# Kernel optimization log

Measured on AMD Instinct MI355X. Metric: run time of the kernel, lower is better.

The kernel has to match this reference:

```python
import jax, jax.numpy as jnp
import numpy as np

R, K = 16, 64  # rel_size (heads), key_size (head dim)
LN_EPS = 1e-5


def apply_rope(x, pos):
    # pos: [B,S,1,K], halves are sin/cos; x: [B,S,R,K]
    sin, cos = jnp.split(pos, 2, axis=-1)
    x0, x1 = jnp.split(x, 2, axis=-1)
    return jnp.concatenate([x0 * cos - x1 * sin, x0 * sin + x1 * cos], axis=-1)


def setup_inputs() -> dict:
    key = jax.random.key(0)
    ks = jax.random.split(key, 6)
    B, S, H = 2, 2048, 1024
    x = jax.random.normal(ks[0], (B, S, H), dtype=jnp.float32)
    pos = jax.random.uniform(ks[1], (B, S, 1, K), dtype=jnp.float32)
    W_qkv = jax.random.normal(ks[2], (H, R * K * 3), dtype=jnp.float32) * (H ** -0.5)
    b_qkv = jax.random.normal(ks[3], (R * K * 3,), dtype=jnp.float32) * 0.02
    W_out = jax.random.normal(ks[4], (R * K, H), dtype=jnp.float32) * ((R * K) ** -0.5)
    b_out = jax.random.normal(ks[5], (H,), dtype=jnp.float32) * 0.02
    ln_g = jnp.ones((H,), dtype=jnp.float32)
    ln_b = jnp.zeros((H,), dtype=jnp.float32)
    return {"x": x, "pos": pos, "W_qkv": W_qkv, "b_qkv": b_qkv,
            "W_out": W_out, "b_out": b_out, "ln_g": ln_g, "ln_b": ln_b}


def reference(x, pos, W_qkv, b_qkv, W_out, b_out, ln_g, ln_b):
    B, S, H = x.shape
    qkv = (x @ W_qkv + b_qkv).reshape(B, S, R, 3 * K)
    q, k, v = jnp.split(qkv, 3, axis=-1)  # each [B,S,R,K]
    k = k / jnp.linalg.norm(k, axis=-1, keepdims=True)
    q = apply_rope(q, pos)
    k = apply_rope(k, pos)
    # SDPA with scale=1 (as in the original call)
    scores = jnp.einsum('bqhd,bkhd->bhqk', q, k)
    attn = jax.nn.softmax(scores, axis=-1)
    ctx = jnp.einsum('bhqk,bkhd->bqhd', attn, v).reshape(B, S, R * K)
    postx = ctx @ W_out + b_out
    y = x + postx
    mu = jnp.mean(y, axis=-1, keepdims=True)
    var = jnp.mean(jnp.square(y - mu), axis=-1, keepdims=True)
    return (y - mu) * jax.lax.rsqrt(var + LN_EPS) * ln_g + ln_b
```

## Files before the change

### kernel.cpp

```cpp
#include <hip/hip_runtime.h>


#define B_   2
#define S_   2048
#define H_   1024
#define R_   16
#define BS_  (B_*S_)
#define NQKV 3072
#define LOG2E 1.44269504088896f

typedef float    floatx4 __attribute__((ext_vector_type(4)));
typedef _Float16 half8   __attribute__((ext_vector_type(8)));
typedef _Float16 half4   __attribute__((ext_vector_type(4)));
typedef __fp16   fp16x2  __attribute__((ext_vector_type(2)));

#if __has_builtin(__builtin_amdgcn_exp2f)
#define EXP2(x) __builtin_amdgcn_exp2f(x)
#else
#define EXP2(x) exp2f(x)
#endif

__device__ __forceinline__ void gl_lds16(const _Float16* g, _Float16* l) {
    __builtin_amdgcn_global_load_lds(
        (const __attribute__((address_space(1))) unsigned int*)g,
        (__attribute__((address_space(3))) unsigned int*)l, 16, 0, 0);
}

__global__ __launch_bounds__(256) void prep0_kernel(
    const float* __restrict__ x, _Float16* __restrict__ x_h,
    const float* __restrict__ W_qkv, _Float16* __restrict__ wqkv_t,
    const float* __restrict__ W_out, _Float16* __restrict__ wout_t)
{
    __shared__ float tile[32][33];
    int bid = blockIdx.x, tid = threadIdx.x;
    if (bid < 4096) {
        int i = bid * 1024 + tid * 4;
        float4 v = *(const float4*)(x + i);
        half4 h;
        h.x = (_Float16)v.x; h.y = (_Float16)v.y;
        h.z = (_Float16)v.z; h.w = (_Float16)v.w;
        *(half4*)(x_h + i) = h;
        return;
    }
    const float* in; _Float16* out; int rows, cols, bx, by;
    if (bid < 7168) {
        int t = bid - 4096;
        in = W_qkv; out = wqkv_t; rows = H_; cols = NQKV;
        bx = t % 96; by = t / 96;
    } else {
        int t = bid - 7168;
        in = W_out; out = wout_t; rows = H_; cols = H_;
        bx = t & 31; by = t >> 5;
    }
    int cx = bx * 32, ry = by * 32;
    int tx = tid & 31, ty = tid >> 5;
#pragma unroll
    for (int i = 0; i < 32; i += 8)
        tile[ty + i][tx] = in[(size_t)(ry + ty + i) * cols + cx + tx];
    __syncthreads();
#pragma unroll
    for (int i = 0; i < 32; i += 8)
        out[(size_t)(cx + ty + i) * rows + ry + tx] = (_Float16)tile[tx][ty + i];
}

__global__ __launch_bounds__(256) void gemm_f16_mfma(
    const _Float16* __restrict__ A, const _Float16* __restrict__ Bt,
    const float* __restrict__ bias, _Float16* __restrict__ Ch,
    int M, int N, int Kd)
{
    __shared__ _Float16 Als[2][4096];
    __shared__ _Float16 Bls[2][4096];
    int tid  = threadIdx.x;
    int lane = tid & 63, w = tid >> 6;
    int wr = w >> 1, wc = w & 1;
    int fr = lane & 15, fq = lane >> 4;

    int nbx = gridDim.x;
    int orig = blockIdx.x + nbx * blockIdx.y;
    int nwg  = nbx * gridDim.y;
    int swz  = (nwg & 7) ? orig : ((orig & 7) * (nwg >> 3) + (orig >> 3));
    int bx = swz % nbx, by = swz / nbx;
    int m0 = by * 128, n0 = bx * 128;

    floatx4 acc[4][4] = {};

    const _Float16* ga[2]; const _Float16* gb[2];
    int loff[2];
#pragma unroll
    for (int i2 = 0; i2 < 2; ++i2) {
        int ch = 2 * w + i2;
        int row = ch * 16 + (lane >> 2), col = (lane & 3) * 8;
        ga[i2] = A  + (size_t)(m0 + row) * Kd + col;
        gb[i2] = Bt + (size_t)(n0 + row) * Kd + col;
        loff[i2] = ch * 512;
    }

    int nIter = Kd >> 5;
#pragma unroll
    for (int i2 = 0; i2 < 2; ++i2) {
        gl_lds16(ga[i2], &Als[0][loff[i2]]);
        gl_lds16(gb[i2], &Bls[0][loff[i2]]);
    }

    for (int it = 0; it < nIter; ++it) {
        int cur = it & 1;
        __syncthreads();
        if (it + 1 < nIter) {
            int k1 = (it + 1) << 5;
#pragma unroll
            for (int i2 = 0; i2 < 2; ++i2) {
                gl_lds16(ga[i2] + k1, &Als[cur ^ 1][loff[i2]]);
                gl_lds16(gb[i2] + k1, &Bls[cur ^ 1][loff[i2]]);
            }
        }
        const _Float16* Ab = Als[cur];
        const _Float16* Bb = Bls[cur];
        half8 af[4], bf[4];
#pragma unroll
        for (int i = 0; i < 4; ++i)
            af[i] = *(const half8*)(Ab + (wr * 64 + i * 16 + fr) * 32 + fq * 8);
#pragma unroll
        for (int j = 0; j < 4; ++j)
            bf[j] = *(const half8*)(Bb + (wc * 64 + j * 16 + fr) * 32 + fq * 8);
#pragma unroll
        for (int i = 0; i < 4; ++i)
#pragma unroll
            for (int j = 0; j < 4; ++j)
                acc[i][j] = __builtin_amdgcn_mfma_f32_16x16x32_f16(
                    af[i], bf[j], acc[i][j], 0, 0, 0);
    }

#pragma unroll
    for (int i = 0; i < 4; ++i)
#pragma unroll
        for (int j = 0; j < 4; ++j)
#pragma unroll
            for (int r2 = 0; r2 < 4; ++r2) {
                int row = m0 + wr * 64 + i * 16 + fq * 4 + r2;
                int col = n0 + wc * 64 + j * 16 + fr;
                Ch[(size_t)row * N + col] = (_Float16)(acc[i][j][r2] + bias[col]);
            }
}

__global__ __launch_bounds__(256) void gemm64_f16_mfma(
    const _Float16* __restrict__ A, const _Float16* __restrict__ Bt,
    const float* __restrict__ bias, const float* __restrict__ resid,
    float* __restrict__ Cf, int M, int N, int Kd)
{
    __shared__ _Float16 Als[2][2048];
    __shared__ _Float16 Bls[2][2048];
    int tid = threadIdx.x, lane = tid & 63, w = tid >> 6;
    int wr = w >> 1, wc = w & 1;
    int fr = lane & 15, fq = lane >> 4;

    int nbx = gridDim.x;
    int orig = blockIdx.x + nbx * blockIdx.y;
    int nwg  = nbx * gridDim.y;
    int swz  = (nwg & 7) ? orig : ((orig & 7) * (nwg >> 3) + (orig >> 3));
    int bx = swz % nbx, by = swz / nbx;
    int m0 = by * 64, n0 = bx * 64;

    floatx4 acc[2][2] = {};

    int srow = w * 16 + (lane >> 2), scol = (lane & 3) * 8;
    const _Float16* ga = A  + (size_t)(m0 + srow) * Kd + scol;
    const _Float16* gb = Bt + (size_t)(n0 + srow) * Kd + scol;
    int loff = w * 512;

    int nIter = Kd >> 5;
    gl_lds16(ga, &Als[0][loff]);
    gl_lds16(gb, &Bls[0][loff]);

    for (int it = 0; it < nIter; ++it) {
        int cur = it & 1;
        __syncthreads();
        if (it + 1 < nIter) {
            int k1 = (it + 1) << 5;
            gl_lds16(ga + k1, &Als[cur ^ 1][loff]);
            gl_lds16(gb + k1, &Bls[cur ^ 1][loff]);
        }
        const _Float16* Ab = Als[cur];
        const _Float16* Bb = Bls[cur];
        half8 af[2], bf[2];
#pragma unroll
        for (int i = 0; i < 2; ++i)
            af[i] = *(const half8*)(Ab + (wr * 32 + i * 16 + fr) * 32 + fq * 8);
#pragma unroll
        for (int j = 0; j < 2; ++j)
            bf[j] = *(const half8*)(Bb + (wc * 32 + j * 16 + fr) * 32 + fq * 8);
#pragma unroll
        for (int i = 0; i < 2; ++i)
#pragma unroll
            for (int j = 0; j < 2; ++j)
                acc[i][j] = __builtin_amdgcn_mfma_f32_16x16x32_f16(
                    af[i], bf[j], acc[i][j], 0, 0, 0);
    }

#pragma unroll
    for (int i = 0; i < 2; ++i)
#pragma unroll
        for (int j = 0; j < 2; ++j)
#pragma unroll
            for (int r2 = 0; r2 < 4; ++r2) {
                int row = m0 + wr * 32 + i * 16 + fq * 4 + r2;
                int col = n0 + wc * 32 + j * 16 + fr;
                Cf[(size_t)row * N + col] =
                    acc[i][j][r2] + bias[col] + resid[(size_t)row * N + col];
            }
}

__global__ __launch_bounds__(256) void prep1_kernel(
    const _Float16* __restrict__ qkvh, const float* __restrict__ pos,
    _Float16* __restrict__ qt, _Float16* __restrict__ kt,
    _Float16* __restrict__ vt2)
{
    __shared__ float tile[64][65];
    int head = blockIdx.x, tau = blockIdx.y;
    int s0 = tau * 64;
    int b = head >> 4, rh = head & 15;
    int lane = threadIdx.x & 63, w = threadIdx.x >> 6;

#pragma unroll
    for (int si = w; si < 64; si += 4)
        tile[si][lane] =
            (float)qkvh[(size_t)(b * S_ + s0 + si) * NQKV + rh * 192 + 128 + lane];
    __syncthreads();
    {
        int P = lane;
        int op = P >> 3;
        int hi = (P >> 2) & 1, lo = P & 3;
#pragma unroll
        for (int d = w; d < 64; d += 4) {
            int ol = op ^ (d & 7);
            int key = 32 * (ol >> 2) + 16 * hi + 4 * (ol & 3) + lo;
            vt2[(((size_t)head * 32 + tau) * 64 + d) * 64 + P] = (_Float16)tile[key][d];
        }
    }

    for (int i = 0; i < 16; ++i) {
        int s = s0 + w * 16 + i;
        int bs = b * S_ + s;
        const _Float16* base = qkvh + (size_t)bs * NQKV + rh * 192;
        float qv = (float)base[lane];
        float kv = (float)base[64 + lane];

        float ss = kv * kv;
#pragma unroll
        for (int off = 32; off > 0; off >>= 1) ss += __shfl_xor(ss, off);
        kv *= rsqrtf(ss);

        int j = lane & 31;
        float sn = pos[(size_t)bs * 64 + j];
        float cs = pos[(size_t)bs * 64 + 32 + j];
        float qp = __shfl_xor(qv, 32);
        float kp = __shfl_xor(kv, 32);
        float qo, ko;
        if (lane < 32) { qo = qv * cs - qp * sn; ko = kv * cs - kp * sn; }
        else           { qo = qp * sn + qv * cs; ko = kp * sn + kv * cs; }

        size_t oidx = ((size_t)head * S_ + s) * 64 + lane;
        qt[oidx] = (_Float16)(qo * LOG2E);
        kt[oidx] = (_Float16)ko;
    }
}

__global__ __launch_bounds__(256) void attn_mfma_kernel(
    const _Float16* __restrict__ qt, const _Float16* __restrict__ kt,
    const _Float16* __restrict__ vt2,
    _Float16* __restrict__ opart, float* __restrict__ lpart)
{
    __shared__ _Float16 Kls[2][4096];
    __shared__ _Float16 Vls[2][4096];

    int orig = blockIdx.x + 16 * blockIdx.y + 512 * blockIdx.z;
    int swz  = (orig & 7) * 128 + (orig >> 3);
    int q0   = (swz & 15) * 128;
    int head = (swz >> 4) & 31;
    int ks   = swz >> 9;

    int b = head >> 4, rh = head & 15;
    int tid = threadIdx.x, lane = tid & 63, w = tid >> 6;
    int g = lane >> 4, c = lane & 15;

    half8 qf[2][2];
    float mL[2], l_s[2] = {0.f, 0.f};
#pragma unroll
    for (int qg = 0; qg < 2; ++qg) {
        const _Float16* qp =
            qt + ((size_t)head * S_ + q0 + w * 32 + qg * 16 + c) * 64 + 8 * g;
        qf[qg][0] = *(const half8*)qp;
        qf[qg][1] = *(const half8*)(qp + 32);
        float qq = 0.f;
#pragma unroll
        for (int i = 0; i < 8; ++i) {
            float a = (float)qf[qg][0][i], b2 = (float)qf[qg][1][i];
            qq += a * a + b2 * b2;
        }
        qq += __shfl_xor(qq, 16);
        qq += __shfl_xor(qq, 32);
        mL[qg] = sqrtf(qq);
    }

    floatx4 o_acc[2][4] = {};

    const _Float16* kg[2]; const _Float16* vg[2];
    int loff[2];
#pragma unroll
    for (int i2 = 0; i2 < 2; ++i2) {
        int ch = 2 * w + i2;
        int krow = ch * 8 + (lane >> 3);
        int koct = (lane & 7) ^ (lane >> 3);
        kg[i2] = kt + ((size_t)head * S_ + krow) * 64 + koct * 8;
        vg[i2] = vt2 + ((size_t)head * 32) * 4096 + ch * 512 + lane * 8;
        loff[i2] = ch * 512;
    }

    int co = c & 7;
    int jbase = ks << 4;

#pragma unroll
    for (int i2 = 0; i2 < 2; ++i2) {
        gl_lds16(kg[i2] + (size_t)jbase * 4096, &Kls[0][loff[i2]]);
        gl_lds16(vg[i2] + (size_t)jbase * 4096, &Vls[0][loff[i2]]);
    }

    for (int jt = 0; jt < 16; ++jt) {
        int cur = jt & 1;
        __syncthreads();
        if (jt + 1 < 16) {
            size_t joff = (size_t)(jbase + jt + 1) * 4096;
#pragma unroll
            for (int i2 = 0; i2 < 2; ++i2) {
                gl_lds16(kg[i2] + joff, &Kls[cur ^ 1][loff[i2]]);
                gl_lds16(vg[i2] + joff, &Vls[cur ^ 1][loff[i2]]);
            }
        }
        const _Float16* Kbuf = Kls[cur];
        const _Float16* Vbuf = Vls[cur];

        half8 kfr[8];
#pragma unroll
        for (int t = 0; t < 4; ++t) {
            const _Float16* krow = Kbuf + (16 * t + c) * 64;
            kfr[2 * t]     = *(const half8*)(krow + ((g) ^ co) * 8);
            kfr[2 * t + 1] = *(const half8*)(krow + ((4 + g) ^ co) * 8);
        }

        union { half8 v; fp16x2 h2[4]; } pf[2][2];
#pragma unroll
        for (int qg = 0; qg < 2; ++qg) {
            floatx4 sacc[4];
#pragma unroll
            for (int t = 0; t < 4; ++t) {
                floatx4 z = {};
                z = __builtin_amdgcn_mfma_f32_16x16x32_f16(
                    kfr[2 * t], qf[qg][0], z, 0, 0, 0);
                z = __builtin_amdgcn_mfma_f32_16x16x32_f16(
                    kfr[2 * t + 1], qf[qg][1], z, 0, 0, 0);
                sacc[t] = z;
            }
            float mLq = mL[qg], ps = 0.f;
#pragma unroll
            for (int t = 0; t < 4; ++t)
#pragma unroll
                for (int r = 0; r < 4; ++r) {
                    float p = EXP2(sacc[t][r] - mLq);
                    sacc[t][r] = p;
                    ps += p;
                }
            l_s[qg] += ps;
            pf[qg][0].h2[0] = __builtin_amdgcn_cvt_pkrtz(sacc[0][0], sacc[0][1]);
            pf[qg][0].h2[1] = __builtin_amdgcn_cvt_pkrtz(sacc[0][2], sacc[0][3]);
            pf[qg][0].h2[2] = __builtin_amdgcn_cvt_pkrtz(sacc[1][0], sacc[1][1]);
            pf[qg][0].h2[3] = __builtin_amdgcn_cvt_pkrtz(sacc[1][2], sacc[1][3]);
            pf[qg][1].h2[0] = __builtin_amdgcn_cvt_pkrtz(sacc[2][0], sacc[2][1]);
            pf[qg][1].h2[1] = __builtin_amdgcn_cvt_pkrtz(sacc[2][2], sacc[2][3]);
            pf[qg][1].h2[2] = __builtin_amdgcn_cvt_pkrtz(sacc[3][0], sacc[3][1]);
            pf[qg][1].h2[3] = __builtin_amdgcn_cvt_pkrtz(sacc[3][2], sacc[3][3]);
        }

#pragma unroll
        for (int t = 0; t < 4; ++t) {
            const _Float16* vrow = Vbuf + (16 * t + c) * 64;
            half8 v0 = *(const half8*)(vrow + ((g) ^ co) * 8);
            half8 v1 = *(const half8*)(vrow + ((4 + g) ^ co) * 8);
#pragma unroll
            for (int qg = 0; qg < 2; ++qg) {
                o_acc[qg][t] = __builtin_amdgcn_mfma_f32_16x16x32_f16(
                    v0, pf[qg][0].v, o_acc[qg][t], 0, 0, 0);
                o_acc[qg][t] = __builtin_amdgcn_mfma_f32_16x16x32_f16(
                    v1, pf[qg][1].v, o_acc[qg][t], 0, 0, 0);
            }
        }
    }

#pragma unroll
    for (int qg = 0; qg < 2; ++qg) {
        float lt = l_s[qg];
        lt += __shfl_xor(lt, 16);
        lt += __shfl_xor(lt, 32);
        int q = q0 + w * 32 + qg * 16 + c;
        if (lane < 16)
            lpart[((size_t)ks * 32 + head) * S_ + q] = lt;
        size_t rowbase =
            ((size_t)ks * BS_ + (size_t)(b * S_ + q)) * 1024 + rh * 64;
#pragma unroll
        for (int t = 0; t < 4; ++t) {
            union { half4 v; fp16x2 h2[2]; } e;
            e.h2[0] = __builtin_amdgcn_cvt_pkrtz(o_acc[qg][t][0], o_acc[qg][t][1]);
            e.h2[1] = __builtin_amdgcn_cvt_pkrtz(o_acc[qg][t][2], o_acc[qg][t][3]);
            *(half4*)(opart + rowbase + 16 * t + 4 * g) = e.v;
        }
    }
}

__global__ __launch_bounds__(256) void merge_kernel(
    const _Float16* __restrict__ opart, const float* __restrict__ lpart,
    _Float16* __restrict__ ctx)
{
    int idx = blockIdx.x * 256 + threadIdx.x;
    int row = idx >> 7;
    int col = (idx & 127) * 8;
    int b = row >> 11, s = row & 2047;
    int head = b * 16 + (col >> 6);
    float l0 = lpart[(size_t)head * S_ + s];
    float l1 = lpart[(size_t)(32 + head) * S_ + s];
    float inv = 1.f / (l0 + l1);
    size_t off = (size_t)row * 1024 + col;
    half8 a = *(const half8*)(opart + off);
    half8 b8 = *(const half8*)(opart + (size_t)BS_ * 1024 + off);
    union { half8 v; fp16x2 h2[4]; } e;
#pragma unroll
    for (int i = 0; i < 4; ++i)
        e.h2[i] = __builtin_amdgcn_cvt_pkrtz(
            ((float)a[2 * i]     + (float)b8[2 * i])     * inv,
            ((float)a[2 * i + 1] + (float)b8[2 * i + 1]) * inv);
    *(half8*)(ctx + off) = e.v;
}

__global__ __launch_bounds__(256) void ln_kernel(
    float* __restrict__ y, const float* __restrict__ g, const float* __restrict__ bb)
{
    int row = blockIdx.x, tid = threadIdx.x;
    float* p = y + (size_t)row * 1024;
    float4 v = ((const float4*)p)[tid];
    float sum = v.x + v.y + v.z + v.w;
    float sq  = v.x*v.x + v.y*v.y + v.z*v.z + v.w*v.w;
#pragma unroll
    for (int off = 32; off > 0; off >>= 1) {
        sum += __shfl_xor(sum, off);
        sq  += __shfl_xor(sq,  off);
    }
    __shared__ float rs[4], rq[4];
    int w = tid >> 6;
    if ((tid & 63) == 0) { rs[w] = sum; rq[w] = sq; }
    __syncthreads();
    sum = rs[0] + rs[1] + rs[2] + rs[3];
    sq  = rq[0] + rq[1] + rq[2] + rq[3];
    float mean = sum * (1.f / 1024.f);
    float var  = sq * (1.f / 1024.f) - mean * mean;
    float inv  = rsqrtf(var + 1e-5f);
    float4 gv = ((const float4*)g)[tid];
    float4 bv = ((const float4*)bb)[tid];
    v.x = (v.x - mean) * inv * gv.x + bv.x;
    v.y = (v.y - mean) * inv * gv.y + bv.y;
    v.z = (v.z - mean) * inv * gv.z + bv.z;
    v.w = (v.w - mean) * inv * gv.w + bv.w;
    ((float4*)p)[tid] = v;
}

extern "C" void kernel_launch(void* const* d_in, const int* in_sizes, int n_in,
                              void* d_out, int out_size, void* d_ws, size_t ws_size,
                              hipStream_t stream)
{
    const float* x     = (const float*)d_in[0];
    const float* pos   = (const float*)d_in[1];
    const float* W_qkv = (const float*)d_in[2];
    const float* b_qkv = (const float*)d_in[3];
    const float* W_out = (const float*)d_in[4];
    const float* b_out = (const float*)d_in[5];
    const float* ln_g  = (const float*)d_in[6];
    const float* ln_b  = (const float*)d_in[7];
    float* out = (float*)d_out;

    char* ws = (char*)d_ws;
    _Float16* x_h    = (_Float16*)(ws);
    _Float16* ctx_h  = (_Float16*)(ws);
    _Float16* wqkv_t = (_Float16*)(ws + ((size_t)8  << 20));
    _Float16* wout_t = (_Float16*)(ws + ((size_t)14 << 20));
    _Float16* qkvh   = (_Float16*)(ws + ((size_t)16 << 20));
    _Float16* opart  = (_Float16*)(ws + ((size_t)16 << 20));
    float*    lpart  = (float*)   (ws + ((size_t)32 << 20));
    _Float16* qt_h   = (_Float16*)(ws + ((size_t)40 << 20));
    _Float16* kt_h   = (_Float16*)(ws + ((size_t)48 << 20));
    _Float16* vt2_h  = (_Float16*)(ws + ((size_t)56 << 20));

    prep0_kernel<<<8192, 256, 0, stream>>>(x, x_h, W_qkv, wqkv_t, W_out, wout_t);

    gemm_f16_mfma<<<dim3(NQKV / 128, BS_ / 128), 256, 0, stream>>>(
        x_h, wqkv_t, b_qkv, qkvh, BS_, NQKV, H_);

    prep1_kernel<<<dim3(32, 32), 256, 0, stream>>>(qkvh, pos, qt_h, kt_h, vt2_h);

    attn_mfma_kernel<<<dim3(16, 32, 2), 256, 0, stream>>>(
        qt_h, kt_h, vt2_h, opart, lpart);

    merge_kernel<<<2048, 256, 0, stream>>>(opart, lpart, ctx_h);

    gemm64_f16_mfma<<<dim3(H_ / 64, BS_ / 64), 256, 0, stream>>>(
        ctx_h, wout_t, b_out, x, out, BS_, H_, H_);

    ln_kernel<<<BS_, 256, 0, stream>>>(out, ln_g, ln_b);
}
```

Baseline: 224.7 us.

## Split attention KV range four ways and add MFMA priority hints

Raises the key-split count from 2 to 4, so each attention block covers 8 key tiles instead of 16 and the grid doubles to 2048 blocks. The merge kernel now sums four partial outputs and four partial row sums. s_setprio wraps the MFMA sections so waves issuing matrix work get scheduler priority. The workspace is reshuffled so the larger opart buffer (four 8 MB slices) fits. The cost is more partial-output traffic and more merge work in exchange for more parallelism and shorter per-block loops.

```diff
diff --git a/kernel.cpp b/kernel.cpp
--- a/kernel.cpp
+++ b/kernel.cpp
@@ -7,6 +7,7 @@
 #define R_   16
 #define BS_  (B_*S_)
 #define NQKV 3072
+#define NSPLIT 4
 #define LOG2E 1.44269504088896f
 
 typedef float    floatx4 __attribute__((ext_vector_type(4)));
@@ -273,7 +274,7 @@
     __shared__ _Float16 Vls[2][4096];
 
     int orig = blockIdx.x + 16 * blockIdx.y + 512 * blockIdx.z;
-    int swz  = (orig & 7) * 128 + (orig >> 3);
+    int swz  = (orig & 7) * 256 + (orig >> 3);
     int q0   = (swz & 15) * 128;
     int head = (swz >> 4) & 31;
     int ks   = swz >> 9;
@@ -316,7 +317,7 @@
     }
 
     int co = c & 7;
-    int jbase = ks << 4;
+    int jbase = ks << 3;
 
 #pragma unroll
     for (int i2 = 0; i2 < 2; ++i2) {
@@ -324,10 +325,10 @@
         gl_lds16(vg[i2] + (size_t)jbase * 4096, &Vls[0][loff[i2]]);
     }
 
-    for (int jt = 0; jt < 16; ++jt) {
+    for (int jt = 0; jt < 8; ++jt) {
         int cur = jt & 1;
         __syncthreads();
-        if (jt + 1 < 16) {
+        if (jt + 1 < 8) {
             size_t joff = (size_t)(jbase + jt + 1) * 4096;
 #pragma unroll
             for (int i2 = 0; i2 < 2; ++i2) {
@@ -350,6 +351,7 @@
 #pragma unroll
         for (int qg = 0; qg < 2; ++qg) {
             floatx4 sacc[4];
+            __builtin_amdgcn_s_setprio(1);
 #pragma unroll
             for (int t = 0; t < 4; ++t) {
                 floatx4 z = {};
@@ -359,6 +361,7 @@
                     kfr[2 * t + 1], qf[qg][1], z, 0, 0, 0);
                 sacc[t] = z;
             }
+            __builtin_amdgcn_s_setprio(0);
             float mLq = mL[qg], ps = 0.f;
 #pragma unroll
             for (int t = 0; t < 4; ++t)
@@ -379,6 +382,7 @@
             pf[qg][1].h2[3] = __builtin_amdgcn_cvt_pkrtz(sacc[3][2], sacc[3][3]);
         }
 
+        __builtin_amdgcn_s_setprio(1);
 #pragma unroll
         for (int t = 0; t < 4; ++t) {
             const _Float16* vrow = Vbuf + (16 * t + c) * 64;
@@ -392,6 +396,7 @@
                     v1, pf[qg][1].v, o_acc[qg][t], 0, 0, 0);
             }
         }
+        __builtin_amdgcn_s_setprio(0);
     }
 
 #pragma unroll
@@ -423,18 +428,23 @@
     int col = (idx & 127) * 8;
     int b = row >> 11, s = row & 2047;
     int head = b * 16 + (col >> 6);
-    float l0 = lpart[(size_t)head * S_ + s];
-    float l1 = lpart[(size_t)(32 + head) * S_ + s];
-    float inv = 1.f / (l0 + l1);
+    float lsum = 0.f;
+#pragma unroll
+    for (int i = 0; i < NSPLIT; ++i)
+        lsum += lpart[((size_t)i * 32 + head) * S_ + s];
+    float inv = 1.f / lsum;
     size_t off = (size_t)row * 1024 + col;
-    half8 a = *(const half8*)(opart + off);
-    half8 b8 = *(const half8*)(opart + (size_t)BS_ * 1024 + off);
+    float acc[8] = {};
+#pragma unroll
+    for (int i = 0; i < NSPLIT; ++i) {
+        half8 a = *(const half8*)(opart + (size_t)i * BS_ * 1024 + off);
+#pragma unroll
+        for (int j = 0; j < 8; ++j) acc[j] += (float)a[j];
+    }
     union { half8 v; fp16x2 h2[4]; } e;
 #pragma unroll
     for (int i = 0; i < 4; ++i)
-        e.h2[i] = __builtin_amdgcn_cvt_pkrtz(
-            ((float)a[2 * i]     + (float)b8[2 * i])     * inv,
-            ((float)a[2 * i + 1] + (float)b8[2 * i + 1]) * inv);
+        e.h2[i] = __builtin_amdgcn_cvt_pkrtz(acc[2 * i] * inv, acc[2 * i + 1] * inv);
     *(half8*)(ctx + off) = e.v;
 }
 
@@ -485,15 +495,15 @@
 
     char* ws = (char*)d_ws;
     _Float16* x_h    = (_Float16*)(ws);
-    _Float16* ctx_h  = (_Float16*)(ws);
     _Float16* wqkv_t = (_Float16*)(ws + ((size_t)8  << 20));
-    _Float16* wout_t = (_Float16*)(ws + ((size_t)14 << 20));
-    _Float16* qkvh   = (_Float16*)(ws + ((size_t)16 << 20));
-    _Float16* opart  = (_Float16*)(ws + ((size_t)16 << 20));
+    _Float16* qkvh   = (_Float16*)(ws + ((size_t)14 << 20));
+    _Float16* opart  = (_Float16*)(ws);
     float*    lpart  = (float*)   (ws + ((size_t)32 << 20));
-    _Float16* qt_h   = (_Float16*)(ws + ((size_t)40 << 20));
-    _Float16* kt_h   = (_Float16*)(ws + ((size_t)48 << 20));
-    _Float16* vt2_h  = (_Float16*)(ws + ((size_t)56 << 20));
+    _Float16* ctx_h  = (_Float16*)(ws + ((size_t)33 << 20));
+    _Float16* qt_h   = (_Float16*)(ws + ((size_t)38 << 20));
+    _Float16* kt_h   = (_Float16*)(ws + ((size_t)46 << 20));
+    _Float16* vt2_h  = (_Float16*)(ws + ((size_t)54 << 20));
+    _Float16* wout_t = (_Float16*)(ws + ((size_t)62 << 20));
 
     prep0_kernel<<<8192, 256, 0, stream>>>(x, x_h, W_qkv, wqkv_t, W_out, wout_t);
 
@@ -502,7 +512,7 @@
 
     prep1_kernel<<<dim3(32, 32), 256, 0, stream>>>(qkvh, pos, qt_h, kt_h, vt2_h);
 
-    attn_mfma_kernel<<<dim3(16, 32, 2), 256, 0, stream>>>(
+    attn_mfma_kernel<<<dim3(16, 32, NSPLIT), 256, 0, stream>>>(
         qt_h, kt_h, vt2_h, opart, lpart);
 
     merge_kernel<<<2048, 256, 0, stream>>>(opart, lpart, ctx_h);
```

After: 243.5 us. +8.4%, slower.

## Load K and V fragments directly from global memory instead of LDS staging

Applied to the files above, without the earlier changes.

Removes the double-buffered LDS staging of K and V tiles (global_load_lds plus __syncthreads) in the attention kernel, so each wave reads its MFMA fragments straight from global memory and relies on the cache. This drops the barriers and the LDS footprint, which may raise occupancy. The cost is that the four waves each re-read the same K/V tile from L2 with no explicit prefetch, so load latency is no longer overlapped. The V read keeps the XOR-swizzled addressing, which matches the vt2 layout only if that buffer was pre-swizzled in global memory.

```diff
diff --git a/kernel.cpp b/kernel.cpp
--- a/kernel.cpp
+++ b/kernel.cpp
@@ -269,9 +269,6 @@
     const _Float16* __restrict__ vt2,
     _Float16* __restrict__ opart, float* __restrict__ lpart)
 {
-    __shared__ _Float16 Kls[2][4096];
-    __shared__ _Float16 Vls[2][4096];
-
     int orig = blockIdx.x + 16 * blockIdx.y + 512 * blockIdx.z;
     int swz  = (orig & 7) * 128 + (orig >> 3);
     int q0   = (swz & 15) * 128;
@@ -303,47 +300,21 @@
 
     floatx4 o_acc[2][4] = {};
 
-    const _Float16* kg[2]; const _Float16* vg[2];
-    int loff[2];
-#pragma unroll
-    for (int i2 = 0; i2 < 2; ++i2) {
-        int ch = 2 * w + i2;
-        int krow = ch * 8 + (lane >> 3);
-        int koct = (lane & 7) ^ (lane >> 3);
-        kg[i2] = kt + ((size_t)head * S_ + krow) * 64 + koct * 8;
-        vg[i2] = vt2 + ((size_t)head * 32) * 4096 + ch * 512 + lane * 8;
-        loff[i2] = ch * 512;
-    }
-
     int co = c & 7;
     int jbase = ks << 4;
 
-#pragma unroll
-    for (int i2 = 0; i2 < 2; ++i2) {
-        gl_lds16(kg[i2] + (size_t)jbase * 4096, &Kls[0][loff[i2]]);
-        gl_lds16(vg[i2] + (size_t)jbase * 4096, &Vls[0][loff[i2]]);
-    }
-
     for (int jt = 0; jt < 16; ++jt) {
-        int cur = jt & 1;
-        __syncthreads();
-        if (jt + 1 < 16) {
-            size_t joff = (size_t)(jbase + jt + 1) * 4096;
-#pragma unroll
-            for (int i2 = 0; i2 < 2; ++i2) {
-                gl_lds16(kg[i2] + joff, &Kls[cur ^ 1][loff[i2]]);
-                gl_lds16(vg[i2] + joff, &Vls[cur ^ 1][loff[i2]]);
-            }
-        }
-        const _Float16* Kbuf = Kls[cur];
-        const _Float16* Vbuf = Vls[cur];
+        const _Float16* kb =
+            kt + ((size_t)head * S_ + (size_t)(jbase + jt) * 64) * 64;
+        const _Float16* vb =
+            vt2 + ((size_t)(head * 32) + jbase + jt) * 4096;
 
         half8 kfr[8];
 #pragma unroll
         for (int t = 0; t < 4; ++t) {
-            const _Float16* krow = Kbuf + (16 * t + c) * 64;
-            kfr[2 * t]     = *(const half8*)(krow + ((g) ^ co) * 8);
-            kfr[2 * t + 1] = *(const half8*)(krow + ((4 + g) ^ co) * 8);
+            const _Float16* krow = kb + (16 * t + c) * 64;
+            kfr[2 * t]     = *(const half8*)(krow + g * 8);
+            kfr[2 * t + 1] = *(const half8*)(krow + 32 + g * 8);
         }
 
         union { half8 v; fp16x2 h2[4]; } pf[2][2];
@@ -381,7 +352,7 @@
 
 #pragma unroll
         for (int t = 0; t < 4; ++t) {
-            const _Float16* vrow = Vbuf + (16 * t + c) * 64;
+            const _Float16* vrow = vb + (16 * t + c) * 64;
             half8 v0 = *(const half8*)(vrow + ((g) ^ co) * 8);
             half8 v1 = *(const half8*)(vrow + ((4 + g) ^ co) * 8);
 #pragma unroll
```

Measured after the change: 265.4 us. 1.18x slower.
